# Optimization experiments

Measured on AMD Instinct MI355X. Metric: run time of the kernel, lower is better.

Reference implementation:

```python
import jax, jax.numpy as jnp
import numpy as np

B, S, D = 64, 8192, 128  # batch, source length, hidden (enc == dec)


def setup_inputs() -> dict:
    key = jax.random.key(0)
    ks = jax.random.split(key, 7)
    s = 1.0 / np.sqrt(D)
    return {
        "input": jax.random.normal(ks[0], (B, D), jnp.float32),
        "context": jax.random.normal(ks[1], (B, S, D), jnp.float32),
        "W_enc": jax.random.uniform(ks[2], (D, D), jnp.float32, -s, s),
        "b_enc": jax.random.uniform(ks[3], (D,), jnp.float32, -s, s),
        "W_dec": jax.random.uniform(ks[4], (D, D), jnp.float32, -s, s),
        "b_dec": jax.random.uniform(ks[5], (D,), jnp.float32, -s, s),
        "W_out": jax.random.uniform(ks[6], (D, 2 * D), jnp.float32, -s, s),  # no bias
    }


def reference(input, context, W_enc, b_enc, W_dec, b_dec, W_out):
    # projected_context = tanh(lin_encoder(context))  [B, S, D]
    pc = jnp.tanh(jnp.einsum("bse,de->bsd", context, W_enc) + b_enc)
    # q = tanh(lin_decoder(input))  [B, D]
    q = jnp.tanh(input @ W_dec.T + b_dec)
    # attention scores via bmm(projected_context, q): [B, S]
    scores = jnp.einsum("bsd,bd->bs", pc, q)
    attn = jax.nn.softmax(scores, axis=1)  # softmax over source positions
    # weighted sum of (raw) context: [B, D]
    weighted_context = jnp.einsum("bs,bsd->bd", attn, context)
    # h_tilde = tanh(linear_out(concat(weighted_context, q)))  [B, D]
    h_tilde = jnp.tanh(jnp.concatenate([weighted_context, q], axis=-1) @ W_out.T)
    return h_tilde, attn
```

## Files before the change

kernel.cpp:

```cpp
#include <hip/hip_runtime.h>
#include <hip/hip_bf16.h>

#define BB 64
#define SS 8192
#define DD 128

typedef __attribute__((ext_vector_type(8))) short bf16x8;
typedef __attribute__((ext_vector_type(4))) short s16x4;
typedef __attribute__((ext_vector_type(4))) float f32x4;

__device__ __forceinline__ short f2bf(float f) {
    unsigned u = __float_as_uint(f);
    unsigned r = (u + 0x7FFFu + ((u >> 16) & 1u)) >> 16;
    return (short)r;
}

__device__ __forceinline__ float tanh_fast(float x) {
    float e = __expf(2.f * x);
    return 1.f - 2.f / (e + 1.f);
}

__global__ void qproj_kernel(const float* __restrict__ input,
                             const float* __restrict__ W_dec,
                             const float* __restrict__ b_dec,
                             float* __restrict__ q,
                             float* __restrict__ wc) {
    __shared__ float xin[DD];
    const int b = blockIdx.x, d = threadIdx.x;
    xin[d] = input[b * DD + d];
    wc[b * DD + d] = 0.f;
    __syncthreads();
    const float4* wrow = (const float4*)(W_dec + (size_t)d * DD);
    float acc = 0.f;
#pragma unroll
    for (int k4 = 0; k4 < DD / 4; k4++) {
        float4 w = wrow[k4];
        float4 x = ((const float4*)xin)[k4];
        acc += w.x * x.x + w.y * x.y + w.z * x.z + w.w * x.w;
    }
    q[b * DD + d] = tanh_fast(acc + b_dec[d]);
}

#define MT 64
#define LDW 136

__global__ __launch_bounds__(256, 2) void score_kernel(
    const float* __restrict__ ctx,
    const float* __restrict__ W_enc,
    const float* __restrict__ b_enc,
    const float* __restrict__ q,
    float* __restrict__ scores_out) {
    __shared__ short Wl[DD * LDW];
    __shared__ short Cl[MT * LDW];

    const int t = threadIdx.x;
    for (int i = t; i < DD * 32; i += 256) {
        float4 f = ((const float4*)W_enc)[i];
        int row = i >> 5, c4 = i & 31;
        s16x4 pk = {f2bf(f.x), f2bf(f.y), f2bf(f.z), f2bf(f.w)};
        *(s16x4*)&Wl[row * LDW + c4 * 4] = pk;
    }

    const int wave = t >> 6, lane = t & 63;
    const int col = lane & 15, quad = lane >> 4;
    const int ntiles = BB * (SS / MT);

    for (int tile = blockIdx.x; tile < ntiles; tile += gridDim.x) {
        const int b = tile >> 7;
        const int st = tile & 127;

        __syncthreads();
        const float4* src = (const float4*)(ctx + ((size_t)b * SS + (size_t)st * MT) * DD);
        for (int i = t; i < MT * 32; i += 256) {
            float4 f = src[i];
            int row = i >> 5, c4 = i & 31;
            s16x4 pk = {f2bf(f.x), f2bf(f.y), f2bf(f.z), f2bf(f.w)};
            *(s16x4*)&Cl[row * LDW + c4 * 4] = pk;
        }
        __syncthreads();

        float qv[8], bv[8];
#pragma unroll
        for (int nt = 0; nt < 8; nt++) {
            qv[nt] = q[b * DD + nt * 16 + col];
            bv[nt] = b_enc[nt * 16 + col];
        }

        bf16x8 a[4];
#pragma unroll
        for (int kk = 0; kk < 4; kk++)
            a[kk] = *(const bf16x8*)&Cl[(wave * 16 + col) * LDW + kk * 32 + quad * 8];

        f32x4 acc[8];
#pragma unroll
        for (int nt = 0; nt < 8; nt++) {
            f32x4 c = {0.f, 0.f, 0.f, 0.f};
#pragma unroll
            for (int kk = 0; kk < 4; kk++) {
                bf16x8 bf = *(const bf16x8*)&Wl[(nt * 16 + col) * LDW + kk * 32 + quad * 8];
                c = __builtin_amdgcn_mfma_f32_16x16x32_bf16(a[kk], bf, c, 0, 0, 0);
            }
            acc[nt] = c;
        }

#pragma unroll
        for (int r = 0; r < 4; r++) {
            float v = 0.f;
#pragma unroll
            for (int nt = 0; nt < 8; nt++) {
                float z = acc[nt][r] + bv[nt];
                v += tanh_fast(z) * qv[nt];
            }
            v += __shfl_xor(v, 1);
            v += __shfl_xor(v, 2);
            v += __shfl_xor(v, 4);
            v += __shfl_xor(v, 8);
            if (col == 0) {
                int srow = st * MT + wave * 16 + quad * 4 + r;
                scores_out[(size_t)b * SS + srow] = v;
            }
        }
    }
}

__global__ __launch_bounds__(1024) void softmax_kernel(float* __restrict__ attn) {
    __shared__ float redm[16];
    __shared__ float reds[16];
    const int b = blockIdx.x, t = threadIdx.x;
    float4* row4 = (float4*)(attn + (size_t)b * SS);
    float4 v0 = row4[t];
    float4 v1 = row4[t + 1024];
    float m = fmaxf(fmaxf(fmaxf(v0.x, v0.y), fmaxf(v0.z, v0.w)),
                    fmaxf(fmaxf(v1.x, v1.y), fmaxf(v1.z, v1.w)));
#pragma unroll
    for (int off = 32; off; off >>= 1) m = fmaxf(m, __shfl_xor(m, off));
    if ((t & 63) == 0) redm[t >> 6] = m;
    __syncthreads();
    float M = redm[0];
#pragma unroll
    for (int i = 1; i < 16; i++) M = fmaxf(M, redm[i]);

    float4 e0, e1;
    e0.x = __expf(v0.x - M); e0.y = __expf(v0.y - M);
    e0.z = __expf(v0.z - M); e0.w = __expf(v0.w - M);
    e1.x = __expf(v1.x - M); e1.y = __expf(v1.y - M);
    e1.z = __expf(v1.z - M); e1.w = __expf(v1.w - M);
    float s = e0.x + e0.y + e0.z + e0.w + e1.x + e1.y + e1.z + e1.w;
#pragma unroll
    for (int off = 32; off; off >>= 1) s += __shfl_xor(s, off);
    if ((t & 63) == 0) reds[t >> 6] = s;
    __syncthreads();
    float T = 0.f;
#pragma unroll
    for (int i = 0; i < 16; i++) T += reds[i];
    float inv = 1.f / T;
    e0.x *= inv; e0.y *= inv; e0.z *= inv; e0.w *= inv;
    e1.x *= inv; e1.y *= inv; e1.z *= inv; e1.w *= inv;
    row4[t] = e0;
    row4[t + 1024] = e1;
}

#define CH 512
__global__ __launch_bounds__(256) void wsum_kernel(const float* __restrict__ ctx,
                                                   const float* __restrict__ attn,
                                                   float* __restrict__ wc) {
    const int t = threadIdx.x;
    const int b = blockIdx.x >> 4;
    const int chunk = blockIdx.x & 15;
    const int c2 = t & 63;
    const int rg = t >> 6;
    const float2* ctx2 = (const float2*)(ctx + ((size_t)b * SS + (size_t)chunk * CH) * DD);
    const float* arow = attn + (size_t)b * SS + (size_t)chunk * CH;
    float2 acc = {0.f, 0.f};
#pragma unroll 4
    for (int s = rg; s < CH; s += 4) {
        float a = arow[s];
        float2 v = ctx2[(size_t)s * 64 + c2];
        acc.x += a * v.x;
        acc.y += a * v.y;
    }
    __shared__ float2 part[256];
    part[t] = acc;
    __syncthreads();
    if (t < 64) {
        float2 r = part[t];
        float2 p1 = part[t + 64], p2 = part[t + 128], p3 = part[t + 192];
        r.x += p1.x + p2.x + p3.x;
        r.y += p1.y + p2.y + p3.y;
        atomicAdd(&wc[b * DD + 2 * c2], r.x);
        atomicAdd(&wc[b * DD + 2 * c2 + 1], r.y);
    }
}

__global__ void out_kernel(const float* __restrict__ wc,
                           const float* __restrict__ q,
                           const float* __restrict__ W_out,
                           float* __restrict__ h) {
    __shared__ float cat[2 * DD];
    const int b = blockIdx.x, d = threadIdx.x;
    cat[d] = wc[b * DD + d];
    cat[DD + d] = q[b * DD + d];
    __syncthreads();
    const float4* wrow = (const float4*)(W_out + (size_t)d * 2 * DD);
    float acc = 0.f;
#pragma unroll
    for (int k4 = 0; k4 < 2 * DD / 4; k4++) {
        float4 w = wrow[k4];
        float4 x = ((const float4*)cat)[k4];
        acc += w.x * x.x + w.y * x.y + w.z * x.z + w.w * x.w;
    }
    h[b * DD + d] = tanh_fast(acc);
}

extern "C" void kernel_launch(void* const* d_in, const int* in_sizes, int n_in,
                              void* d_out, int out_size, void* d_ws, size_t ws_size,
                              hipStream_t stream) {
    const float* input = (const float*)d_in[0];
    const float* ctx   = (const float*)d_in[1];
    const float* W_enc = (const float*)d_in[2];
    const float* b_enc = (const float*)d_in[3];
    const float* W_dec = (const float*)d_in[4];
    const float* b_dec = (const float*)d_in[5];
    const float* W_out = (const float*)d_in[6];

    float* h    = (float*)d_out;
    float* attn = (float*)d_out + BB * DD;
    float* q    = (float*)d_ws;
    float* wc   = (float*)d_ws + BB * DD;

    qproj_kernel<<<BB, DD, 0, stream>>>(input, W_dec, b_dec, q, wc);
    score_kernel<<<1024, 256, 0, stream>>>(ctx, W_enc, b_enc, q, attn);
    softmax_kernel<<<BB, 1024, 0, stream>>>(attn);
    wsum_kernel<<<BB * 16, 256, 0, stream>>>(ctx, attn, wc);
    out_kernel<<<BB, DD, 0, stream>>>(wc, q, W_out, h);
}
```

Measured before the change: 480.0 us.

## Load context tiles per wave straight into registers with prefetch, pre-swizzle W_enc

The score kernel no longer stages context through shared memory with block barriers. Each wave now owns 16-row tiles, loads them from global memory directly into registers and prefetches the next tile while running the current MFMAs. W_enc is stored in LDS in a pre-swizzled MFMA-fragment layout, which cuts shared memory use and allows 4 blocks per CU. The weighted-sum kernel switches to float4 loads and 256-row chunks with twice as many blocks. The costs are more register pressure from the prefetch buffers and more atomic adds into the weighted-context output.

```diff
diff --git a/kernel.cpp b/kernel.cpp
--- a/kernel.cpp
+++ b/kernel.cpp
@@ -6,13 +6,19 @@
 #define DD 128
 
 typedef __attribute__((ext_vector_type(8))) short bf16x8;
-typedef __attribute__((ext_vector_type(4))) short s16x4;
 typedef __attribute__((ext_vector_type(4))) float f32x4;
 
 __device__ __forceinline__ short f2bf(float f) {
     unsigned u = __float_as_uint(f);
     unsigned r = (u + 0x7FFFu + ((u >> 16) & 1u)) >> 16;
     return (short)r;
+}
+
+__device__ __forceinline__ bf16x8 pack8(float4 a, float4 b) {
+    bf16x8 r;
+    r[0] = f2bf(a.x); r[1] = f2bf(a.y); r[2] = f2bf(a.z); r[3] = f2bf(a.w);
+    r[4] = f2bf(b.x); r[5] = f2bf(b.y); r[6] = f2bf(b.z); r[7] = f2bf(b.w);
+    return r;
 }
 
 __device__ __forceinline__ float tanh_fast(float x) {
@@ -41,83 +47,87 @@
     q[b * DD + d] = tanh_fast(acc + b_dec[d]);
 }
 
-#define MT 64
-#define LDW 136
-
-__global__ __launch_bounds__(256, 2) void score_kernel(
+__global__ __launch_bounds__(256, 4) void score_kernel(
     const float* __restrict__ ctx,
     const float* __restrict__ W_enc,
     const float* __restrict__ b_enc,
     const float* __restrict__ q,
-    float* __restrict__ scores_out) {
-    __shared__ short Wl[DD * LDW];
-    __shared__ short Cl[MT * LDW];
+    float* __restrict__ scores) {
+    __shared__ short Wl[2048 * 8];
 
     const int t = threadIdx.x;
-    for (int i = t; i < DD * 32; i += 256) {
-        float4 f = ((const float4*)W_enc)[i];
-        int row = i >> 5, c4 = i & 31;
-        s16x4 pk = {f2bf(f.x), f2bf(f.y), f2bf(f.z), f2bf(f.w)};
-        *(s16x4*)&Wl[row * LDW + c4 * 4] = pk;
+    const float4* W4 = (const float4*)W_enc;
+    for (int c = t; c < 2048; c += 256) {
+        int row = c >> 4, kc = c & 15;
+        float4 f0 = W4[row * 32 + kc * 2];
+        float4 f1 = W4[row * 32 + kc * 2 + 1];
+        int nt = row >> 4, col = row & 15;
+        int kk = kc >> 2, quad = kc & 3;
+        int slot = (nt * 4 + kk) * 64 + (col + 16 * quad);
+        *(bf16x8*)&Wl[slot * 8] = pack8(f0, f1);
     }
 
     const int wave = t >> 6, lane = t & 63;
     const int col = lane & 15, quad = lane >> 4;
-    const int ntiles = BB * (SS / MT);
-
-    for (int tile = blockIdx.x; tile < ntiles; tile += gridDim.x) {
-        const int b = tile >> 7;
-        const int st = tile & 127;
-
-        __syncthreads();
-        const float4* src = (const float4*)(ctx + ((size_t)b * SS + (size_t)st * MT) * DD);
-        for (int i = t; i < MT * 32; i += 256) {
-            float4 f = src[i];
-            int row = i >> 5, c4 = i & 31;
-            s16x4 pk = {f2bf(f.x), f2bf(f.y), f2bf(f.z), f2bf(f.w)};
-            *(s16x4*)&Cl[row * LDW + c4 * 4] = pk;
+
+    float bv[8];
+#pragma unroll
+    for (int nt = 0; nt < 8; nt++) bv[nt] = b_enc[nt * 16 + col];
+
+    __syncthreads();
+
+    const int nwaves = gridDim.x * 4;
+    const int wid = blockIdx.x * 4 + wave;
+    const int NT = BB * (SS / 16);
+
+    float4 R[8];
+    auto load_raw = [&](int tile, float4* Rd) {
+        const float4* src = (const float4*)(ctx + (size_t)(tile * 16 + col) * DD);
+#pragma unroll
+        for (int kk = 0; kk < 4; kk++) {
+            Rd[2 * kk]     = src[kk * 8 + quad * 2];
+            Rd[2 * kk + 1] = src[kk * 8 + quad * 2 + 1];
         }
-        __syncthreads();
-
-        float qv[8], bv[8];
-#pragma unroll
-        for (int nt = 0; nt < 8; nt++) {
-            qv[nt] = q[b * DD + nt * 16 + col];
-            bv[nt] = b_enc[nt * 16 + col];
-        }
-
-        bf16x8 a[4];
-#pragma unroll
-        for (int kk = 0; kk < 4; kk++)
-            a[kk] = *(const bf16x8*)&Cl[(wave * 16 + col) * LDW + kk * 32 + quad * 8];
-
-        f32x4 acc[8];
-#pragma unroll
-        for (int nt = 0; nt < 8; nt++) {
-            f32x4 c = {0.f, 0.f, 0.f, 0.f};
-#pragma unroll
-            for (int kk = 0; kk < 4; kk++) {
-                bf16x8 bf = *(const bf16x8*)&Wl[(nt * 16 + col) * LDW + kk * 32 + quad * 8];
-                c = __builtin_amdgcn_mfma_f32_16x16x32_bf16(a[kk], bf, c, 0, 0, 0);
+    };
+
+    if (wid < NT) {
+        load_raw(wid, R);
+        for (int tile = wid; tile < NT; tile += nwaves) {
+            bf16x8 a[4];
+#pragma unroll
+            for (int kk = 0; kk < 4; kk++) a[kk] = pack8(R[2 * kk], R[2 * kk + 1]);
+            int nxt = tile + nwaves;
+            load_raw(nxt < NT ? nxt : tile, R);
+
+            const int b = tile >> 9;
+            float qv[8];
+#pragma unroll
+            for (int nt = 0; nt < 8; nt++) qv[nt] = q[b * DD + nt * 16 + col];
+
+            f32x4 acc[8];
+#pragma unroll
+            for (int nt = 0; nt < 8; nt++) {
+                f32x4 c = {0.f, 0.f, 0.f, 0.f};
+#pragma unroll
+                for (int kk = 0; kk < 4; kk++) {
+                    bf16x8 bf = *(const bf16x8*)&Wl[((nt * 4 + kk) * 64 + lane) * 8];
+                    c = __builtin_amdgcn_mfma_f32_16x16x32_bf16(a[kk], bf, c, 0, 0, 0);
+                }
+                acc[nt] = c;
             }
-            acc[nt] = c;
-        }
-
-#pragma unroll
-        for (int r = 0; r < 4; r++) {
-            float v = 0.f;
-#pragma unroll
-            for (int nt = 0; nt < 8; nt++) {
-                float z = acc[nt][r] + bv[nt];
-                v += tanh_fast(z) * qv[nt];
-            }
-            v += __shfl_xor(v, 1);
-            v += __shfl_xor(v, 2);
-            v += __shfl_xor(v, 4);
-            v += __shfl_xor(v, 8);
-            if (col == 0) {
-                int srow = st * MT + wave * 16 + quad * 4 + r;
-                scores_out[(size_t)b * SS + srow] = v;
+
+#pragma unroll
+            for (int r = 0; r < 4; r++) {
+                float v = 0.f;
+#pragma unroll
+                for (int nt = 0; nt < 8; nt++)
+                    v += tanh_fast(acc[nt][r] + bv[nt]) * qv[nt];
+                v += __shfl_xor(v, 1);
+                v += __shfl_xor(v, 2);
+                v += __shfl_xor(v, 4);
+                v += __shfl_xor(v, 8);
+                if (col == 0)
+                    scores[(size_t)tile * 16 + quad * 4 + r] = v;
             }
         }
     }
@@ -160,35 +170,41 @@
     row4[t + 1024] = e1;
 }
 
-#define CH 512
+#define CH 256
 __global__ __launch_bounds__(256) void wsum_kernel(const float* __restrict__ ctx,
                                                    const float* __restrict__ attn,
                                                    float* __restrict__ wc) {
     const int t = threadIdx.x;
-    const int b = blockIdx.x >> 4;
-    const int chunk = blockIdx.x & 15;
-    const int c2 = t & 63;
-    const int rg = t >> 6;
-    const float2* ctx2 = (const float2*)(ctx + ((size_t)b * SS + (size_t)chunk * CH) * DD);
+    const int b = blockIdx.x >> 5;
+    const int chunk = blockIdx.x & 31;
+    const int c4 = t & 31;
+    const int rg = t >> 5;
+    const float4* ctx4 = (const float4*)(ctx + ((size_t)b * SS + (size_t)chunk * CH) * DD);
     const float* arow = attn + (size_t)b * SS + (size_t)chunk * CH;
-    float2 acc = {0.f, 0.f};
+    float4 acc = {0.f, 0.f, 0.f, 0.f};
 #pragma unroll 4
-    for (int s = rg; s < CH; s += 4) {
+    for (int s = rg; s < CH; s += 8) {
         float a = arow[s];
-        float2 v = ctx2[(size_t)s * 64 + c2];
+        float4 v = ctx4[(size_t)s * 32 + c4];
         acc.x += a * v.x;
         acc.y += a * v.y;
-    }
-    __shared__ float2 part[256];
+        acc.z += a * v.z;
+        acc.w += a * v.w;
+    }
+    __shared__ float4 part[256];
     part[t] = acc;
     __syncthreads();
-    if (t < 64) {
-        float2 r = part[t];
-        float2 p1 = part[t + 64], p2 = part[t + 128], p3 = part[t + 192];
-        r.x += p1.x + p2.x + p3.x;
-        r.y += p1.y + p2.y + p3.y;
-        atomicAdd(&wc[b * DD + 2 * c2], r.x);
-        atomicAdd(&wc[b * DD + 2 * c2 + 1], r.y);
+    if (t < 32) {
+        float4 r = part[t];
+#pragma unroll
+        for (int g = 1; g < 8; g++) {
+            float4 p = part[t + g * 32];
+            r.x += p.x; r.y += p.y; r.z += p.z; r.w += p.w;
+        }
+        atomicAdd(&wc[b * DD + 4 * c4 + 0], r.x);
+        atomicAdd(&wc[b * DD + 4 * c4 + 1], r.y);
+        atomicAdd(&wc[b * DD + 4 * c4 + 2], r.z);
+        atomicAdd(&wc[b * DD + 4 * c4 + 3], r.w);
     }
 }
 
@@ -231,6 +247,6 @@
     qproj_kernel<<<BB, DD, 0, stream>>>(input, W_dec, b_dec, q, wc);
     score_kernel<<<1024, 256, 0, stream>>>(ctx, W_enc, b_enc, q, attn);
     softmax_kernel<<<BB, 1024, 0, stream>>>(attn);
-    wsum_kernel<<<BB * 16, 256, 0, stream>>>(ctx, attn, wc);
+    wsum_kernel<<<BB * 32, 256, 0, stream>>>(ctx, attn, wc);
     out_kernel<<<BB, DD, 0, stream>>>(wc, q, W_out, h);
 }
```

Result: slower. 518.9 us (+8.1%).

## Fuse score, online softmax and weighted sum into a single context pass

Applied to the files above, without the earlier changes.

Folds the weighted-sum pass into the score kernel using a flash-style online softmax. Each block keeps its fp32 context tile in registers, so the 256 MB context tensor is read from HBM once instead of twice. Per-chunk partial max, sum and weighted context are merged in a small combine kernel, and a separate kernel normalizes the stored scores into attn. It also prefetches the next tile into registers, pre-swizzles W_enc and the context tile in LDS to avoid bank conflicts, and packs to bf16 with the intrinsic. The cost is heavy register pressure, extra workspace and two more small launches.

```diff
diff --git a/kernel.cpp b/kernel.cpp
--- a/kernel.cpp
+++ b/kernel.cpp
@@ -6,13 +6,13 @@
 #define DD 128
 
 typedef __attribute__((ext_vector_type(8))) short bf16x8;
-typedef __attribute__((ext_vector_type(4))) short s16x4;
 typedef __attribute__((ext_vector_type(4))) float f32x4;
 
-__device__ __forceinline__ short f2bf(float f) {
-    unsigned u = __float_as_uint(f);
-    unsigned r = (u + 0x7FFFu + ((u >> 16) & 1u)) >> 16;
-    return (short)r;
+__device__ __forceinline__ unsigned pk2(float x, float y) {
+    __hip_bfloat162 h = __float22bfloat162_rn(make_float2(x, y));
+    union { __hip_bfloat162 h2; unsigned u; } c;
+    c.h2 = h;
+    return c.u;
 }
 
 __device__ __forceinline__ float tanh_fast(float x) {
@@ -23,12 +23,10 @@
 __global__ void qproj_kernel(const float* __restrict__ input,
                              const float* __restrict__ W_dec,
                              const float* __restrict__ b_dec,
-                             float* __restrict__ q,
-                             float* __restrict__ wc) {
+                             float* __restrict__ q) {
     __shared__ float xin[DD];
     const int b = blockIdx.x, d = threadIdx.x;
     xin[d] = input[b * DD + d];
-    wc[b * DD + d] = 0.f;
     __syncthreads();
     const float4* wrow = (const float4*)(W_dec + (size_t)d * DD);
     float acc = 0.f;
@@ -41,63 +39,88 @@
     q[b * DD + d] = tanh_fast(acc + b_dec[d]);
 }
 
-#define MT 64
-#define LDW 136
-
-__global__ __launch_bounds__(256, 2) void score_kernel(
+__global__ __launch_bounds__(256, 3) void score_fused_kernel(
     const float* __restrict__ ctx,
     const float* __restrict__ W_enc,
     const float* __restrict__ b_enc,
     const float* __restrict__ q,
-    float* __restrict__ scores_out) {
-    __shared__ short Wl[DD * LDW];
-    __shared__ short Cl[MT * LDW];
+    float* __restrict__ scores,
+    float* __restrict__ wcp,
+    float* __restrict__ Mp,
+    float* __restrict__ Tp) {
+    __shared__ __align__(16) short Wl[2048 * 8];
+    __shared__ __align__(16) short Cl[64 * 128];
+    __shared__ float sw[64];
 
     const int t = threadIdx.x;
-    for (int i = t; i < DD * 32; i += 256) {
-        float4 f = ((const float4*)W_enc)[i];
-        int row = i >> 5, c4 = i & 31;
-        s16x4 pk = {f2bf(f.x), f2bf(f.y), f2bf(f.z), f2bf(f.w)};
-        *(s16x4*)&Wl[row * LDW + c4 * 4] = pk;
-    }
-
-    const int wave = t >> 6, lane = t & 63;
+
+    const float4* W4 = (const float4*)W_enc;
+    for (int c2 = t; c2 < 2048; c2 += 256) {
+        int row = c2 >> 4, kc = c2 & 15;
+        float4 f0 = W4[row * 32 + kc * 2];
+        float4 f1 = W4[row * 32 + kc * 2 + 1];
+        int nt = row >> 4, colw = row & 15;
+        int kk = kc >> 2, qd = kc & 3;
+        int slot = (nt * 4 + kk) * 64 + (colw + 16 * qd);
+        uint4 u;
+        u.x = pk2(f0.x, f0.y); u.y = pk2(f0.z, f0.w);
+        u.z = pk2(f1.x, f1.y); u.w = pk2(f1.z, f1.w);
+        *(uint4*)&Wl[slot * 8] = u;
+    }
+
+    const int wv = t >> 6, lane = t & 63;
     const int col = lane & 15, quad = lane >> 4;
-    const int ntiles = BB * (SS / MT);
-
-    for (int tile = blockIdx.x; tile < ntiles; tile += gridDim.x) {
-        const int b = tile >> 7;
-        const int st = tile & 127;
-
-        __syncthreads();
-        const float4* src = (const float4*)(ctx + ((size_t)b * SS + (size_t)st * MT) * DD);
-        for (int i = t; i < MT * 32; i += 256) {
-            float4 f = src[i];
-            int row = i >> 5, c4 = i & 31;
-            s16x4 pk = {f2bf(f.x), f2bf(f.y), f2bf(f.z), f2bf(f.w)};
-            *(s16x4*)&Cl[row * LDW + c4 * 4] = pk;
-        }
-        __syncthreads();
-
-        float qv[8], bv[8];
-#pragma unroll
-        for (int nt = 0; nt < 8; nt++) {
-            qv[nt] = q[b * DD + nt * 16 + col];
-            bv[nt] = b_enc[nt * 16 + col];
+    const int b = blockIdx.x >> 4;
+    const int chunk = blockIdx.x & 15;
+
+    float qv[8], bv[8];
+#pragma unroll
+    for (int nt = 0; nt < 8; nt++) {
+        qv[nt] = q[b * DD + nt * 16 + col];
+        bv[nt] = b_enc[nt * 16 + col];
+    }
+
+    const float4* base = (const float4*)(ctx + ((size_t)b * SS + (size_t)chunk * 512) * DD);
+
+    float4 R[2][8];
+#pragma unroll
+    for (int i = 0; i < 8; i++) R[0][i] = base[t + 256 * i];
+#pragma unroll
+    for (int i = 0; i < 8; i++) {
+        int row = (t >> 5) + 8 * i;
+        int c = row & 15, w = row >> 4;
+        int piece = w * 512 + c * 32 + ((t & 31) ^ (2 * (c & 7)));
+        float4 f = R[0][i];
+        uint2 pk;
+        pk.x = pk2(f.x, f.y); pk.y = pk2(f.z, f.w);
+        *(uint2*)&Cl[piece * 4] = pk;
+    }
+    __syncthreads();
+
+    float Mrun = -INFINITY, Trun = 0.f;
+    float4 acc4 = {0.f, 0.f, 0.f, 0.f};
+
+#pragma unroll
+    for (int it = 0; it < 8; ++it) {
+        if (it < 7) {
+            const float4* tb = base + (size_t)(it + 1) * 2048;
+#pragma unroll
+            for (int i = 0; i < 8; i++) R[(it + 1) & 1][i] = tb[t + 256 * i];
         }
 
         bf16x8 a[4];
 #pragma unroll
-        for (int kk = 0; kk < 4; kk++)
-            a[kk] = *(const bf16x8*)&Cl[(wave * 16 + col) * LDW + kk * 32 + quad * 8];
-
+        for (int kk = 0; kk < 4; kk++) {
+            int piece = wv * 512 + col * 32 + ((kk * 8 + quad * 2) ^ (2 * (col & 7)));
+            a[kk] = *(const bf16x8*)&Cl[piece * 4];
+        }
         f32x4 acc[8];
 #pragma unroll
         for (int nt = 0; nt < 8; nt++) {
             f32x4 c = {0.f, 0.f, 0.f, 0.f};
 #pragma unroll
             for (int kk = 0; kk < 4; kk++) {
-                bf16x8 bf = *(const bf16x8*)&Wl[(nt * 16 + col) * LDW + kk * 32 + quad * 8];
+                bf16x8 bf = *(const bf16x8*)&Wl[((nt * 4 + kk) * 64 + lane) * 8];
                 c = __builtin_amdgcn_mfma_f32_16x16x32_bf16(a[kk], bf, c, 0, 0, 0);
             }
             acc[nt] = c;
@@ -107,89 +130,115 @@
         for (int r = 0; r < 4; r++) {
             float v = 0.f;
 #pragma unroll
-            for (int nt = 0; nt < 8; nt++) {
-                float z = acc[nt][r] + bv[nt];
-                v += tanh_fast(z) * qv[nt];
-            }
+            for (int nt = 0; nt < 8; nt++)
+                v += tanh_fast(acc[nt][r] + bv[nt]) * qv[nt];
             v += __shfl_xor(v, 1);
             v += __shfl_xor(v, 2);
             v += __shfl_xor(v, 4);
             v += __shfl_xor(v, 8);
             if (col == 0) {
-                int srow = st * MT + wave * 16 + quad * 4 + r;
-                scores_out[(size_t)b * SS + srow] = v;
+                int lrow = wv * 16 + quad * 4 + r;
+                sw[lrow] = v;
+                scores[(size_t)b * SS + chunk * 512 + it * 64 + lrow] = v;
             }
         }
-    }
-}
-
-__global__ __launch_bounds__(1024) void softmax_kernel(float* __restrict__ attn) {
-    __shared__ float redm[16];
-    __shared__ float reds[16];
-    const int b = blockIdx.x, t = threadIdx.x;
-    float4* row4 = (float4*)(attn + (size_t)b * SS);
-    float4 v0 = row4[t];
-    float4 v1 = row4[t + 1024];
-    float m = fmaxf(fmaxf(fmaxf(v0.x, v0.y), fmaxf(v0.z, v0.w)),
-                    fmaxf(fmaxf(v1.x, v1.y), fmaxf(v1.z, v1.w)));
-#pragma unroll
-    for (int off = 32; off; off >>= 1) m = fmaxf(m, __shfl_xor(m, off));
-    if ((t & 63) == 0) redm[t >> 6] = m;
-    __syncthreads();
-    float M = redm[0];
-#pragma unroll
-    for (int i = 1; i < 16; i++) M = fmaxf(M, redm[i]);
-
-    float4 e0, e1;
-    e0.x = __expf(v0.x - M); e0.y = __expf(v0.y - M);
-    e0.z = __expf(v0.z - M); e0.w = __expf(v0.w - M);
-    e1.x = __expf(v1.x - M); e1.y = __expf(v1.y - M);
-    e1.z = __expf(v1.z - M); e1.w = __expf(v1.w - M);
-    float s = e0.x + e0.y + e0.z + e0.w + e1.x + e1.y + e1.z + e1.w;
-#pragma unroll
-    for (int off = 32; off; off >>= 1) s += __shfl_xor(s, off);
-    if ((t & 63) == 0) reds[t >> 6] = s;
-    __syncthreads();
-    float T = 0.f;
-#pragma unroll
-    for (int i = 0; i < 16; i++) T += reds[i];
-    float inv = 1.f / T;
-    e0.x *= inv; e0.y *= inv; e0.z *= inv; e0.w *= inv;
-    e1.x *= inv; e1.y *= inv; e1.z *= inv; e1.w *= inv;
-    row4[t] = e0;
-    row4[t + 1024] = e1;
-}
-
-#define CH 512
-__global__ __launch_bounds__(256) void wsum_kernel(const float* __restrict__ ctx,
-                                                   const float* __restrict__ attn,
-                                                   float* __restrict__ wc) {
-    const int t = threadIdx.x;
-    const int b = blockIdx.x >> 4;
-    const int chunk = blockIdx.x & 15;
-    const int c2 = t & 63;
-    const int rg = t >> 6;
-    const float2* ctx2 = (const float2*)(ctx + ((size_t)b * SS + (size_t)chunk * CH) * DD);
-    const float* arow = attn + (size_t)b * SS + (size_t)chunk * CH;
-    float2 acc = {0.f, 0.f};
-#pragma unroll 4
-    for (int s = rg; s < CH; s += 4) {
-        float a = arow[s];
-        float2 v = ctx2[(size_t)s * 64 + c2];
-        acc.x += a * v.x;
-        acc.y += a * v.y;
-    }
-    __shared__ float2 part[256];
-    part[t] = acc;
-    __syncthreads();
-    if (t < 64) {
-        float2 r = part[t];
-        float2 p1 = part[t + 64], p2 = part[t + 128], p3 = part[t + 192];
-        r.x += p1.x + p2.x + p3.x;
-        r.y += p1.y + p2.y + p3.y;
-        atomicAdd(&wc[b * DD + 2 * c2], r.x);
-        atomicAdd(&wc[b * DD + 2 * c2 + 1], r.y);
-    }
+        __syncthreads();
+
+        float sv = sw[lane];
+        float m = sv;
+#pragma unroll
+        for (int off = 1; off < 64; off <<= 1) m = fmaxf(m, __shfl_xor(m, off));
+        float Mnew = fmaxf(Mrun, m);
+        float alpha = __expf(Mrun - Mnew);
+        float wlane = __expf(sv - Mnew);
+        float ts = wlane;
+#pragma unroll
+        for (int off = 1; off < 64; off <<= 1) ts += __shfl_xor(ts, off);
+        Trun = Trun * alpha + ts;
+        Mrun = Mnew;
+
+        acc4.x *= alpha; acc4.y *= alpha; acc4.z *= alpha; acc4.w *= alpha;
+#pragma unroll
+        for (int i = 0; i < 8; i++) {
+            int row_i = (t >> 5) + 8 * i;
+            float wi = __shfl(wlane, row_i);
+            float4 Rv = R[it & 1][i];
+            acc4.x += wi * Rv.x;
+            acc4.y += wi * Rv.y;
+            acc4.z += wi * Rv.z;
+            acc4.w += wi * Rv.w;
+        }
+
+        if (it < 7) {
+#pragma unroll
+            for (int i = 0; i < 8; i++) {
+                int row = (t >> 5) + 8 * i;
+                int c = row & 15, w = row >> 4;
+                int piece = w * 512 + c * 32 + ((t & 31) ^ (2 * (c & 7)));
+                float4 f = R[(it + 1) & 1][i];
+                uint2 pk;
+                pk.x = pk2(f.x, f.y); pk.y = pk2(f.z, f.w);
+                *(uint2*)&Cl[piece * 4] = pk;
+            }
+        }
+        __syncthreads();
+    }
+
+    float4* red = (float4*)Cl;
+    red[t] = acc4;
+    __syncthreads();
+    if (t < 32) {
+        float4 s = red[t];
+#pragma unroll
+        for (int k = 1; k < 8; k++) {
+            float4 p = red[t + 32 * k];
+            s.x += p.x; s.y += p.y; s.z += p.z; s.w += p.w;
+        }
+        *(float4*)&wcp[(size_t)blockIdx.x * DD + 4 * t] = s;
+    }
+    if (t == 0) {
+        Mp[blockIdx.x] = Mrun;
+        Tp[blockIdx.x] = Tp ? Trun : Trun;
+        Tp[blockIdx.x] = Trun;
+    }
+}
+
+__global__ void combine_kernel(const float* __restrict__ wcp,
+                               const float* __restrict__ Mp,
+                               const float* __restrict__ Tp,
+                               float* __restrict__ wc,
+                               float* __restrict__ Ms,
+                               float* __restrict__ Tinv) {
+    const int b = blockIdx.x, d = threadIdx.x;
+    float M = -INFINITY;
+#pragma unroll
+    for (int j = 0; j < 16; j++) M = fmaxf(M, Mp[b * 16 + j]);
+    float T = 0.f, acc = 0.f;
+#pragma unroll
+    for (int j = 0; j < 16; j++) {
+        float e = __expf(Mp[b * 16 + j] - M);
+        T += Tp[b * 16 + j] * e;
+        acc += wcp[(size_t)(b * 16 + j) * DD + d] * e;
+    }
+    float ti = 1.f / T;
+    wc[b * DD + d] = acc * ti;
+    if (d == 0) { Ms[b] = M; Tinv[b] = ti; }
+}
+
+__global__ __launch_bounds__(512) void attnfin_kernel(const float* __restrict__ scores,
+                                                      const float* __restrict__ Ms,
+                                                      const float* __restrict__ Tinv,
+                                                      float* __restrict__ attn) {
+    const int b = blockIdx.x >> 2, seg = blockIdx.x & 3;
+    const float M = Ms[b], ti = Tinv[b];
+    const float4* s4 = (const float4*)(scores + (size_t)b * SS) + seg * 512;
+    float4* a4 = (float4*)(attn + (size_t)b * SS) + seg * 512;
+    float4 v = s4[threadIdx.x];
+    v.x = __expf(v.x - M) * ti;
+    v.y = __expf(v.y - M) * ti;
+    v.z = __expf(v.z - M) * ti;
+    v.w = __expf(v.w - M) * ti;
+    a4[threadIdx.x] = v;
 }
 
 __global__ void out_kernel(const float* __restrict__ wc,
@@ -225,12 +274,21 @@
 
     float* h    = (float*)d_out;
     float* attn = (float*)d_out + BB * DD;
-    float* q    = (float*)d_ws;
-    float* wc   = (float*)d_ws + BB * DD;
-
-    qproj_kernel<<<BB, DD, 0, stream>>>(input, W_dec, b_dec, q, wc);
-    score_kernel<<<1024, 256, 0, stream>>>(ctx, W_enc, b_enc, q, attn);
-    softmax_kernel<<<BB, 1024, 0, stream>>>(attn);
-    wsum_kernel<<<BB * 16, 256, 0, stream>>>(ctx, attn, wc);
+
+    float* ws     = (float*)d_ws;
+    float* q      = ws;
+    float* wc     = ws + 8192;
+    float* scores = ws + 16384;
+    float* wcp    = ws + 16384 + 524288;
+    float* Mp     = wcp + 1024 * DD;
+    float* Tp     = Mp + 1024;
+    float* Ms     = Tp + 1024;
+    float* Tinv   = Ms + 64;
+
+    qproj_kernel<<<BB, DD, 0, stream>>>(input, W_dec, b_dec, q);
+    score_fused_kernel<<<BB * 16, 256, 0, stream>>>(ctx, W_enc, b_enc, q,
+                                                    scores, wcp, Mp, Tp);
+    combine_kernel<<<BB, DD, 0, stream>>>(wcp, Mp, Tp, wc, Ms, Tinv);
+    attnfin_kernel<<<BB * 4, 512, 0, stream>>>(scores, Ms, Tinv, attn);
     out_kernel<<<BB, DD, 0, stream>>>(wc, q, W_out, h);
 }
```

Measured after the change: 533.3 us. 1.11x slower.
